# Performance work log

Measured on AMD Instinct MI355X. Metric: run time of the kernel, lower is better.

Reference implementation:

```python
import jax, jax.numpy as jnp
import numpy as np

B, T = 16384, 512          # batch, seq_len
DSTATE, DINPUT = 4, 4       # quaternion state / quaternion input
DMLP1, DMLP2 = 128, 128     # ODEFunc MLP hidden widths


def _linear_params(key, fan_in, fan_out):
    # torch nn.Linear default init: U(-1/sqrt(fan_in), 1/sqrt(fan_in))
    lim = 1.0 / np.sqrt(fan_in)
    kw, kb = jax.random.split(key)
    W = jax.random.uniform(kw, (fan_in, fan_out), jnp.float32, -lim, lim)
    b = jax.random.uniform(kb, (fan_out,), jnp.float32, -lim, lim)
    return W, b


def setup_inputs() -> dict:
    key = jax.random.key(0)
    k1, k2, k3, kx = jax.random.split(key, 4)
    W1, b1 = _linear_params(k1, DSTATE + DINPUT, DMLP1)
    W2, b2 = _linear_params(k2, DMLP1, DMLP2)
    W3, b3 = _linear_params(k3, DMLP2, DSTATE)
    quat_seq = jax.random.normal(kx, (B, T, DINPUT), jnp.float32)
    return {"quat_seq": quat_seq, "W1": W1, "b1": b1, "W2": W2, "b2": b2,
            "W3": W3, "b3": b3}


def reference(quat_seq, W1, b1, W2, b2, W3, b3):
    batch = quat_seq.shape[0]
    dstate = W3.shape[1]

    def odefunc(h, q):
        # f(t, [h, q]) -> dh/dt ; time is unused by the net
        x = jnp.concatenate([h, q], axis=-1)            # [B, DSTATE+DINPUT]
        x = jax.nn.silu(x @ W1 + b1)                    # [B, DMLP1]
        x = jax.nn.silu(x @ W2 + b2)                    # [B, DMLP2]
        return x @ W3 + b3                              # [B, DSTATE]

    dt = 1.0  # t_span = [0, 1] on a fixed grid -> single RK4 step of size 1

    def step(h, q_t):
        # torchdiffeq fixed-grid 'rk4' uses the 3/8-rule (rk4_alt_step_func)
        k1 = odefunc(h, q_t)
        k2 = odefunc(h + dt * k1 / 3.0, q_t)
        k3 = odefunc(h + dt * (k2 - k1 / 3.0), q_t)
        k4 = odefunc(h + dt * (k1 - k2 + k3), q_t)
        h_new = h + dt * (k1 + 3.0 * (k2 + k3) + k4) / 8.0
        return h_new, None

    h0 = jnp.zeros((batch, dstate), quat_seq.dtype).at[:, 0].set(1.0)
    # scan over time: [T, B, DINPUT]
    h_final, _ = jax.lax.scan(step, h0, jnp.swapaxes(quat_seq, 0, 1))
    return h_final
```

## Files before the change

kernel.cpp:

```cpp
#include <hip/hip_runtime.h>
#include <hip/hip_bf16.h>

typedef float f32x4  __attribute__((ext_vector_type(4)));
typedef float f32x16 __attribute__((ext_vector_type(16)));
typedef short short8v __attribute__((ext_vector_type(8)));
typedef unsigned int uint;

constexpr int TSTEPS = 512;

union FragU { uint u[4]; short8v v; };

__device__ __forceinline__ float silu_f(float x) {
    return __fdividef(x, 1.0f + __expf(-x));
}

__device__ __forceinline__ uint bf16_rne(float x) {
    uint ux = __float_as_uint(x);
    return (ux + 0x7FFFu + ((ux >> 16) & 1u)) & 0xFFFF0000u;
}
__device__ __forceinline__ void split2u(float x, uint &h, uint &l) {
    h = bf16_rne(x);
    float rem = x - __uint_as_float(h);
    l = bf16_rne(rem);
}

__device__ __forceinline__ uint cvtpk(float a, float b) {
    union { __hip_bfloat162 h; uint u; } cv;
    cv.h = __float22bfloat162_rn(make_float2(a, b));
    return cv.u;
}
__device__ __forceinline__ void split4_pk(const f32x4 v, uint2 &hi, uint2 &lo) {
    hi.x = cvtpk(v.x, v.y);
    hi.y = cvtpk(v.z, v.w);
    float h0 = __uint_as_float(hi.x << 16);
    float h1 = __uint_as_float(hi.x & 0xFFFF0000u);
    float h2 = __uint_as_float(hi.y << 16);
    float h3 = __uint_as_float(hi.y & 0xFFFF0000u);
    lo.x = cvtpk(v.x - h0, v.y - h1);
    lo.y = cvtpk(v.z - h2, v.w - h3);
}

#define SX1(lev,kt,gk,b) (((((lev)*8+(kt))*2+(gk))*32+(b))*8)

__global__ __launch_bounds__(256, 2)
void odernn_v10(const float* __restrict__ quat,
                const float* __restrict__ W1, const float* __restrict__ b1,
                const float* __restrict__ W2, const float* __restrict__ b2,
                const float* __restrict__ W3, const float* __restrict__ b3,
                float* __restrict__ out)
{
    __shared__ short sx1[2 * 8 * 2 * 32 * 8];
    __shared__ float sb1[128];
    __shared__ float sb2[128];
    __shared__ float sk3[4][32][4];

    const int tid  = threadIdx.x;
    const int w    = tid >> 6;
    const int lane = tid & 63;
    const int b    = lane & 31;
    const int gp   = lane >> 5;
    const int rowbase = blockIdx.x * 32;

    if (tid < 128) { sb1[tid] = b1[tid]; sb2[tid] = b2[tid]; }

    short8v A2[8][2];
#pragma unroll
    for (int kt = 0; kt < 8; ++kt) {
#pragma unroll
        for (int e = 0; e < 8; ++e) {
            float x = W2[(16 * kt + 8 * gp + e) * 128 + (32 * w + b)];
            uint h2_, l2_; split2u(x, h2_, l2_);
            A2[kt][0][e] = (short)(h2_ >> 16);
            A2[kt][1][e] = (short)(l2_ >> 16);
        }
    }
    short8v A1;
#pragma unroll
    for (int e = 0; e < 8; ++e) {
        float x = W1[e * 128 + (32 * w + b)];
        uint h1_, l1_; split2u(x, h1_, l1_);
        A1[e] = (short)((gp ? l1_ : h1_) >> 16);
    }
    f32x4 W3r[16];
#pragma unroll
    for (int i = 0; i < 16; ++i) {
        const int j = 32 * w + 8 * (i >> 2) + (i & 3) + 4 * gp;
        W3r[i] = *(const f32x4*)&W3[j * 4];
    }
    f32x4 b3v = *(const f32x4*)b3;

    __syncthreads();

    f32x4 h  = {1.0f, 0, 0, 0};
    f32x4 k1 = {0,0,0,0}, k2 = {0,0,0,0}, k3v = {0,0,0,0};
    const float* qp = quat + (size_t)(rowbase + b) * TSTEPS * 4;

    f32x4 qnext = *(const f32x4*)qp;

#pragma unroll 1
    for (int t = 0; t < TSTEPS; ++t) {
        const f32x4 q = qnext;
        const int tn = (t + 1 < TSTEPS) ? t + 1 : t;
        qnext = *(const f32x4*)(qp + 4 * tn);

        uint2 qhi, qlo;
        split4_pk(q, qhi, qlo);
        f32x4 hnew = {0,0,0,0};

#pragma unroll
        for (int s = 0; s < 4; ++s) {
            f32x4 hs = h;
            if (s == 1)      hs += k1 * (1.0f/3.0f);
            else if (s == 2) hs += k2 - k1 * (1.0f/3.0f);
            else if (s == 3) hs += k1 - k2 + k3v;

            uint2 hhi, hlo;
            split4_pk(hs, hhi, hlo);
            FragU b0a, b0b;
            b0a.u[0] = gp ? hlo.x : hhi.x;  b0a.u[1] = gp ? hlo.y : hhi.y;
            b0a.u[2] = gp ? qlo.x : qhi.x;  b0a.u[3] = gp ? qlo.y : qhi.y;
            b0b.u[0] = gp ? hhi.x : hlo.x;  b0b.u[1] = gp ? hhi.y : hlo.y;
            b0b.u[2] = gp ? qhi.x : qlo.x;  b0b.u[3] = gp ? qhi.y : qlo.y;

            f32x16 c1;
#pragma unroll
            for (int qd = 0; qd < 4; ++qd) {
                f32x4 bv = *(const f32x4*)&sb1[32 * w + 8 * qd + 4 * gp];
                c1[4*qd+0] = bv.x; c1[4*qd+1] = bv.y;
                c1[4*qd+2] = bv.z; c1[4*qd+3] = bv.w;
            }
            c1 = __builtin_amdgcn_mfma_f32_32x32x16_bf16(A1, b0a.v, c1, 0, 0, 0);
            c1 = __builtin_amdgcn_mfma_f32_32x32x16_bf16(A1, b0b.v, c1, 0, 0, 0);

#pragma unroll
            for (int qd = 0; qd < 4; ++qd) {
                f32x4 sv;
                sv.x = silu_f(c1[4*qd+0]); sv.y = silu_f(c1[4*qd+1]);
                sv.z = silu_f(c1[4*qd+2]); sv.w = silu_f(c1[4*qd+3]);
                uint2 phi, plo;
                split4_pk(sv, phi, plo);
                const int kt = 2 * w + (qd >> 1);
                const int gk = qd & 1;
                *(uint2*)&sx1[SX1(0, kt, gk, b) + 4 * gp] = phi;
                *(uint2*)&sx1[SX1(1, kt, gk, b) + 4 * gp] = plo;
            }
            __syncthreads();

            f32x16 u, vv;
#pragma unroll
            for (int qd = 0; qd < 4; ++qd) {
                f32x4 bv = *(const f32x4*)&sb2[32 * w + 8 * qd + 4 * gp];
                u[4*qd+0] = bv.x; u[4*qd+1] = bv.y;
                u[4*qd+2] = bv.z; u[4*qd+3] = bv.w;
            }
#pragma unroll
            for (int i = 0; i < 16; ++i) vv[i] = 0.0f;
#pragma unroll
            for (int kt = 0; kt < 8; ++kt) {
                short8v Bh = *(const short8v*)&sx1[SX1(0, kt, gp, b)];
                short8v Bl = *(const short8v*)&sx1[SX1(1, kt, gp, b)];
                if (kt & 1) {
                    vv = __builtin_amdgcn_mfma_f32_32x32x16_bf16(A2[kt][1], Bh, vv, 0, 0, 0);
                    vv = __builtin_amdgcn_mfma_f32_32x32x16_bf16(A2[kt][0], Bl, vv, 0, 0, 0);
                    vv = __builtin_amdgcn_mfma_f32_32x32x16_bf16(A2[kt][0], Bh, vv, 0, 0, 0);
                } else {
                    u = __builtin_amdgcn_mfma_f32_32x32x16_bf16(A2[kt][1], Bh, u, 0, 0, 0);
                    u = __builtin_amdgcn_mfma_f32_32x32x16_bf16(A2[kt][0], Bl, u, 0, 0, 0);
                    u = __builtin_amdgcn_mfma_f32_32x32x16_bf16(A2[kt][0], Bh, u, 0, 0, 0);
                }
            }

            f32x4 p = {0.0f, 0.0f, 0.0f, 0.0f};
#pragma unroll
            for (int i = 0; i < 16; ++i) {
                const float xv = silu_f(u[i] + vv[i]);
                p += xv * W3r[i];
            }
            p.x += __shfl_xor(p.x, 32, 64);
            p.y += __shfl_xor(p.y, 32, 64);
            p.z += __shfl_xor(p.z, 32, 64);
            p.w += __shfl_xor(p.w, 32, 64);
            if (lane < 32) *(f32x4*)&sk3[w][lane][0] = p;
            __syncthreads();

            f32x4 ks = b3v;
#pragma unroll
            for (int w2 = 0; w2 < 4; ++w2)
                ks += *(const f32x4*)&sk3[w2][b][0];

            const float wgt = (s == 1 || s == 2) ? 0.375f : 0.125f;
            hnew += ks * wgt;
            if (s == 0)      k1  = ks;
            else if (s == 1) k2  = ks;
            else if (s == 2) k3v = ks;
        }
        h += hnew;
    }

    if (tid < 32)
        *(f32x4*)&out[(size_t)(rowbase + tid) * 4] = h;
}

extern "C" void kernel_launch(void* const* d_in, const int* in_sizes, int n_in,
                              void* d_out, int out_size, void* d_ws, size_t ws_size,
                              hipStream_t stream)
{
    const float* quat = (const float*)d_in[0];
    const float* W1   = (const float*)d_in[1];
    const float* b1   = (const float*)d_in[2];
    const float* W2   = (const float*)d_in[3];
    const float* b2   = (const float*)d_in[4];
    const float* W3   = (const float*)d_in[5];
    const float* b3   = (const float*)d_in[6];
    float* out        = (float*)d_out;

    const int B = in_sizes[0] / (TSTEPS * 4);
    dim3 grid(B / 32), block(256);
    hipLaunchKernelGGL(odernn_v10, grid, block, 0, stream,
                       quat, W1, b1, W2, b2, W3, b3, out);
}
```

Measured before the change: 6.753 ms.

## Use permlane32 swap for half-wave reduction, reorder LDS layout, prioritize MFMA

Replaces the shfl_xor cross-half reductions with v_permlane32_swap inline asm, which avoids LDS-routed bpermute traffic. Interleaves the hi/lo bf16 planes in the shared activation layout, wraps the layer-2 MFMA loop in s_setprio(1)/s_setprio(0), and reuses the wave's own partial sum from registers instead of rereading it from shared memory. These are several small latency cuts on the sequential recurrence's critical path. The inline asm depends on a gfx950-specific instruction, and the p lanes at or above 32 now also hold the full sum, which is harmless.

```diff
diff --git a/kernel.cpp b/kernel.cpp
--- a/kernel.cpp
+++ b/kernel.cpp
@@ -40,16 +40,25 @@
     lo.y = cvtpk(v.z - h2, v.w - h3);
 }
 
-#define SX1(lev,kt,gk,b) (((((lev)*8+(kt))*2+(gk))*32+(b))*8)
+__device__ __forceinline__ float xhalf_sum(float x) {
+    uint a = __float_as_uint(x);
+    uint b;
+    asm("v_mov_b32 %0, %1\n\t"
+        "v_permlane32_swap_b32 %1, %0"
+        : "=&v"(b), "+v"(a));
+    return __uint_as_float(a) + __uint_as_float(b);
+}
+
+#define SXI(kt,gk,lev,bb) (((((kt)*2+(gk))*2+(lev))*32+(bb))*8)
 
 __global__ __launch_bounds__(256, 2)
-void odernn_v10(const float* __restrict__ quat,
+void odernn_v13(const float* __restrict__ quat,
                 const float* __restrict__ W1, const float* __restrict__ b1,
                 const float* __restrict__ W2, const float* __restrict__ b2,
                 const float* __restrict__ W3, const float* __restrict__ b3,
                 float* __restrict__ out)
 {
-    __shared__ short sx1[2 * 8 * 2 * 32 * 8];
+    __shared__ short sx1[8 * 2 * 2 * 32 * 8];
     __shared__ float sb1[128];
     __shared__ float sb2[128];
     __shared__ float sk3[4][32][4];
@@ -141,8 +150,9 @@
                 split4_pk(sv, phi, plo);
                 const int kt = 2 * w + (qd >> 1);
                 const int gk = qd & 1;
-                *(uint2*)&sx1[SX1(0, kt, gk, b) + 4 * gp] = phi;
-                *(uint2*)&sx1[SX1(1, kt, gk, b) + 4 * gp] = plo;
+                const int base = SXI(kt, gk, 0, b) + 4 * gp;
+                *(uint2*)&sx1[base]       = phi;
+                *(uint2*)&sx1[base + 256] = plo;
             }
             __syncthreads();
 
@@ -155,10 +165,12 @@
             }
 #pragma unroll
             for (int i = 0; i < 16; ++i) vv[i] = 0.0f;
+
+            __builtin_amdgcn_s_setprio(1);
 #pragma unroll
             for (int kt = 0; kt < 8; ++kt) {
-                short8v Bh = *(const short8v*)&sx1[SX1(0, kt, gp, b)];
-                short8v Bl = *(const short8v*)&sx1[SX1(1, kt, gp, b)];
+                short8v Bh = *(const short8v*)&sx1[SXI(kt, gp, 0, b)];
+                short8v Bl = *(const short8v*)&sx1[SXI(kt, gp, 1, b)];
                 if (kt & 1) {
                     vv = __builtin_amdgcn_mfma_f32_32x32x16_bf16(A2[kt][1], Bh, vv, 0, 0, 0);
                     vv = __builtin_amdgcn_mfma_f32_32x32x16_bf16(A2[kt][0], Bl, vv, 0, 0, 0);
@@ -169,6 +181,7 @@
                     u = __builtin_amdgcn_mfma_f32_32x32x16_bf16(A2[kt][0], Bh, u, 0, 0, 0);
                 }
             }
+            __builtin_amdgcn_s_setprio(0);
 
             f32x4 p = {0.0f, 0.0f, 0.0f, 0.0f};
 #pragma unroll
@@ -176,17 +189,17 @@
                 const float xv = silu_f(u[i] + vv[i]);
                 p += xv * W3r[i];
             }
-            p.x += __shfl_xor(p.x, 32, 64);
-            p.y += __shfl_xor(p.y, 32, 64);
-            p.z += __shfl_xor(p.z, 32, 64);
-            p.w += __shfl_xor(p.w, 32, 64);
+            p.x = xhalf_sum(p.x);
+            p.y = xhalf_sum(p.y);
+            p.z = xhalf_sum(p.z);
+            p.w = xhalf_sum(p.w);
             if (lane < 32) *(f32x4*)&sk3[w][lane][0] = p;
             __syncthreads();
 
-            f32x4 ks = b3v;
-#pragma unroll
-            for (int w2 = 0; w2 < 4; ++w2)
-                ks += *(const f32x4*)&sk3[w2][b][0];
+            f32x4 ks = b3v + p;
+#pragma unroll
+            for (int i = 1; i < 4; ++i)
+                ks += *(const f32x4*)&sk3[(w + i) & 3][b][0];
 
             const float wgt = (s == 1 || s == 2) ? 0.375f : 0.125f;
             hnew += ks * wgt;
@@ -216,6 +229,6 @@
 
     const int B = in_sizes[0] / (TSTEPS * 4);
     dim3 grid(B / 32), block(256);
-    hipLaunchKernelGGL(odernn_v10, grid, block, 0, stream,
+    hipLaunchKernelGGL(odernn_v13, grid, block, 0, stream,
                        quat, W1, b1, W2, b2, W3, b3, out);
 }
```

Result: no change. 6.711 ms (-0.6%).
